# Kernel tuning notes

Measured on AMD Instinct MI355X. Metric: run time of the kernel, lower is better.

## Reference

```python
import jax, jax.numpy as jnp
import numpy as np

H, D = 16, 64  # heads, dim_head


def _rope(x):
    # x: (b, h, n, d). rotary-embedding-torch style: interleaved pairs, theta=10000.
    n, d = x.shape[-2], x.shape[-1]
    inv_freq = 1.0 / (10000.0 ** (jnp.arange(0, d, 2, dtype=jnp.float32) / d))  # (d/2,)
    ang = jnp.arange(n, dtype=jnp.float32)[:, None] * inv_freq[None, :]  # (n, d/2)
    cos = jnp.repeat(jnp.cos(ang), 2, axis=-1).astype(x.dtype)  # (n, d) interleaved
    sin = jnp.repeat(jnp.sin(ang), 2, axis=-1).astype(x.dtype)
    xp = x.reshape(*x.shape[:-1], d // 2, 2)
    rot = jnp.stack((-xp[..., 1], xp[..., 0]), axis=-1).reshape(x.shape)
    return x * cos + rot * sin


def setup_inputs() -> dict:
    key = jax.random.key(0)
    k1, k2, k3 = jax.random.split(key, 3)
    b, n, dim = 2, 2048, 1024
    inner = H * D
    x = jax.random.normal(k1, (b, n, dim), jnp.float32)
    w_qkv = jax.random.normal(k2, (dim, 3 * inner), jnp.float32) / np.sqrt(dim).astype(np.float32)
    w_out = jax.random.normal(k3, (inner, dim), jnp.float32) / np.sqrt(inner).astype(np.float32)
    b_out = jnp.zeros((dim,), jnp.float32)
    return {"x": x, "w_qkv": w_qkv, "w_out": w_out, "b_out": b_out}


def reference(x, w_qkv, w_out, b_out):
    b, n, _ = x.shape
    qkv = x @ w_qkv  # (b, n, 3*H*D)
    q, k, v = jnp.split(qkv, 3, axis=-1)

    def split_heads(t):
        return t.reshape(b, n, H, D).transpose(0, 2, 1, 3)  # (b, h, n, d)

    q, k, v = split_heads(q), split_heads(k), split_heads(v)
    q = _rope(q)
    k = _rope(k)
    scale = 1.0 / jnp.sqrt(jnp.asarray(D, dtype=x.dtype))
    scores = jnp.einsum('bhqd,bhkd->bhqk', q, k) * scale
    attn = jax.nn.softmax(scores, axis=-1)
    o = jnp.einsum('bhqk,bhkd->bhqd', attn, v)
    o = o.transpose(0, 2, 1, 3).reshape(b, n, H * D)
    return o @ w_out + b_out
```

## Files before the change

kernel.cpp:

```cpp
#include <hip/hip_runtime.h>
#include <math.h>

#define B_    2
#define N_    2048
#define DIM_  1024
#define H_    16
#define D_    64
#define INNER_ 1024
#define QKVC_ 3072

typedef __attribute__((ext_vector_type(8))) short short8;
typedef __attribute__((ext_vector_type(4))) short short4v;
typedef __attribute__((ext_vector_type(4))) float f32x4;
typedef __attribute__((ext_vector_type(4))) float float4v;
typedef _Float16 half8 __attribute__((ext_vector_type(8)));
typedef __fp16 fp16v2 __attribute__((ext_vector_type(2)));

union h8u { short8 s; half8 h; fp16v2 h2[4]; };
static __device__ __forceinline__ half8 s2h(short8 s) { h8u u; u.s = s; return u.h; }

static __device__ __forceinline__ unsigned short f2h(float f) {
    _Float16 h = (_Float16)f;
    unsigned short u;
    __builtin_memcpy(&u, &h, 2);
    return u;
}

static __device__ __forceinline__ void gload16(const void* g, void* l) {
    __builtin_amdgcn_global_load_lds((__attribute__((address_space(1))) void*)(g),
                                     (__attribute__((address_space(3))) void*)(l),
                                     16, 0, 0);
}

__global__ __launch_bounds__(256) void convert_all(const float* __restrict__ X,
                                                   const float* __restrict__ Wq,
                                                   const float* __restrict__ Wo,
                                                   unsigned short* __restrict__ Xh,
                                                   unsigned short* __restrict__ WqT,
                                                   unsigned short* __restrict__ WoT) {
    __shared__ unsigned short Sh[64][65];
    const int blk = blockIdx.x;
    const int tid = threadIdx.x;
    if (blk < 2048) {
        int t = blk * 256 + tid;
        size_t off = (size_t)t * 8;
        float4v a = *(const float4v*)(X + off);
        float4v b = *(const float4v*)(X + off + 4);
        short8 o;
#pragma unroll
        for (int j = 0; j < 4; ++j) {
            o[j]     = (short)f2h(a[j]);
            o[4 + j] = (short)f2h(b[j]);
        }
        *(short8*)(Xh + off) = o;
        return;
    }
    const float* W;
    unsigned short* T;
    int n0, k0, Nw;
    if (blk < 2816) {
        int g = blk - 2048;
        W = Wq; T = WqT; Nw = QKVC_;
        n0 = (g % 48) * 64; k0 = (g / 48) * 64;
    } else {
        int g = blk - 2816;
        W = Wo; T = WoT; Nw = DIM_;
        n0 = (g % 16) * 64; k0 = (g / 16) * 64;
    }
#pragma unroll
    for (int l = 0; l < 16; ++l) {
        int idx = tid + l * 256;
        int r = idx >> 6, c = idx & 63;
        Sh[c][r] = f2h(W[(size_t)(k0 + r) * Nw + n0 + c]);
    }
    __syncthreads();
#pragma unroll
    for (int l = 0; l < 16; ++l) {
        int idx = tid + l * 256;
        int r = idx >> 6, c = idx & 63;
        T[(size_t)(n0 + r) * 1024 + k0 + c] = Sh[r][c];
    }
}

#define GEMM_STAGE64(gA, gB)                                                       \
    {                                                                              \
        int srow = lane >> 3;                                                      \
        int gsw  = ((lane & 7) ^ srow) * 8;                                        \
        _Pragma("unroll") for (int i_ = 0; i_ < 4; ++i_) {                         \
            gload16(gA + (size_t)(m0 + w * 32 + 8 * i_ + srow) * 1024 + k0 + gsw,  \
                    sA + (w * 32 + 8 * i_) * 64);                                  \
            gload16(gB + (size_t)(n0 + w * 32 + 8 * i_ + srow) * 1024 + k0 + gsw,  \
                    sB + (w * 32 + 8 * i_) * 64);                                  \
        }                                                                          \
    }

#define GEMM_BODY64()                                                              \
    half8 af[4][2], bf[4][2];                                                      \
    _Pragma("unroll") for (int f = 0; f < 4; ++f) {                                \
        int arow = (wr + f * 16 + (lane & 15)) * 64;                               \
        int brow = (wc + f * 16 + (lane & 15)) * 64;                               \
        _Pragma("unroll") for (int h = 0; h < 2; ++h) {                            \
            int g = (((lane >> 4) + 4 * h) ^ (lane & 7)) * 8;                      \
            af[f][h] = s2h(*(const short8*)&sA[arow + g]);                         \
            bf[f][h] = s2h(*(const short8*)&sB[brow + g]);                         \
        }                                                                          \
    }                                                                              \
    _Pragma("unroll") for (int i = 0; i < 4; ++i)                                  \
        _Pragma("unroll") for (int j = 0; j < 4; ++j) {                            \
            acc[i][j] = __builtin_amdgcn_mfma_f32_16x16x32_f16(af[i][0], bf[j][0], acc[i][j], 0, 0, 0); \
            acc[i][j] = __builtin_amdgcn_mfma_f32_16x16x32_f16(af[i][1], bf[j][1], acc[i][j], 0, 0, 0); \
        }

#define XCD_REMAP()                                                                \
    const int fblk = blockIdx.y * gridDim.x + blockIdx.x;                          \
    const int per_ = (gridDim.x * gridDim.y) >> 3;                                 \
    const int rf = (fblk & 7) * per_ + (fblk >> 3);                                \
    const int m0 = (rf / gridDim.x) * 128, n0 = (rf % gridDim.x) * 128;

#define QSCALE 0.180336879963f
__global__ __launch_bounds__(256) void qkv_gemm_mfma(const unsigned short* __restrict__ Ah,
                                                     const unsigned short* __restrict__ Bh,
                                                     unsigned short* __restrict__ Qh,
                                                     unsigned short* __restrict__ Kh,
                                                     unsigned short* __restrict__ Vh) {
    __shared__ __align__(16) unsigned short sA[8192], sB[8192];
    const int tid = threadIdx.x;
    const int lane = tid & 63, w = tid >> 6;
    const int wr = (w >> 1) * 64, wc = (w & 1) * 64;
    XCD_REMAP();
    f32x4 acc[4][4] = {};

    for (int k0 = 0; k0 < 1024; k0 += 64) {
        GEMM_STAGE64(Ah, Bh);
        __syncthreads();
        GEMM_BODY64();
        __syncthreads();
    }

    const int seg = n0 >> 10;
    const int parity = lane & 1;

#pragma unroll
    for (int i = 0; i < 4; ++i) {
        int mbase = m0 + wr + i * 16 + (lane >> 4) * 4;
#pragma unroll
        for (int j = 0; j < 4; ++j) {
            int col = n0 + wc + j * 16 + (lane & 15);
            int wcol = col & 1023;
            int h = wcol >> 6, dd = wcol & 63;
            unsigned short* dst = (seg == 0) ? Qh : (seg == 1 ? Kh : Vh);
            if (seg == 2) {
#pragma unroll
                for (int r = 0; r < 4; ++r) {
                    int row = mbase + r;
                    int b = row >> 11, n = row & (N_ - 1);
                    dst[((size_t)(b * H_ + h) * N_ + n) * D_ + dd] = f2h(acc[i][j][r]);
                }
            } else {
                float freq = __builtin_amdgcn_exp2f((float)(dd >> 1) * -0.4152410118f);
#pragma unroll
                for (int r = 0; r < 4; ++r) {
                    int row = mbase + r;
                    int b = row >> 11, n = row & (N_ - 1);
                    float ang = (float)n * freq;
                    float s = __sinf(ang);
                    float c = __cosf(ang);
                    float val = acc[i][j][r];
                    float partner = __shfl_xor(val, 1);
                    float rot = parity ? (val * c + partner * s)
                                       : (val * c - partner * s);
                    if (seg == 0) rot *= QSCALE;
                    dst[((size_t)(b * H_ + h) * N_ + n) * D_ + dd] = f2h(rot);
                }
            }
        }
    }
}

__global__ __launch_bounds__(256) void out_gemm_mfma(const unsigned short* __restrict__ Ah,
                                                     const unsigned short* __restrict__ Bh,
                                                     const float* __restrict__ bias,
                                                     float* __restrict__ C) {
    __shared__ __align__(16) unsigned short sA[8192], sB[4096];
    const int tid = threadIdx.x;
    const int lane = tid & 63, w = tid >> 6;
    const int wr = w * 32;
    const int fblk = blockIdx.y * gridDim.x + blockIdx.x;
    const int per_ = (gridDim.x * gridDim.y) >> 3;
    const int rf = (fblk & 7) * per_ + (fblk >> 3);
    const int m0 = (rf / gridDim.x) * 128, n0 = (rf % gridDim.x) * 64;
    f32x4 acc[2][4] = {};

    for (int k0 = 0; k0 < 1024; k0 += 64) {
        {
            int srow = lane >> 3;
            int gsw  = ((lane & 7) ^ srow) * 8;
#pragma unroll
            for (int i_ = 0; i_ < 4; ++i_)
                gload16(Ah + (size_t)(m0 + w * 32 + 8 * i_ + srow) * 1024 + k0 + gsw,
                        sA + (w * 32 + 8 * i_) * 64);
            gload16(Bh + (size_t)(n0 + w * 8 + srow) * 1024 + k0 + gsw,
                    sB + (w * 8) * 64);
            gload16(Bh + (size_t)(n0 + 32 + w * 8 + srow) * 1024 + k0 + gsw,
                    sB + (32 + w * 8) * 64);
        }
        __syncthreads();
        {
            half8 af[2][2], bf[4][2];
#pragma unroll
            for (int f = 0; f < 2; ++f) {
                int arow = (wr + f * 16 + (lane & 15)) * 64;
#pragma unroll
                for (int h = 0; h < 2; ++h) {
                    int g = (((lane >> 4) + 4 * h) ^ (lane & 7)) * 8;
                    af[f][h] = s2h(*(const short8*)&sA[arow + g]);
                }
            }
#pragma unroll
            for (int j = 0; j < 4; ++j) {
                int brow = (j * 16 + (lane & 15)) * 64;
#pragma unroll
                for (int h = 0; h < 2; ++h) {
                    int g = (((lane >> 4) + 4 * h) ^ (lane & 7)) * 8;
                    bf[j][h] = s2h(*(const short8*)&sB[brow + g]);
                }
            }
#pragma unroll
            for (int i = 0; i < 2; ++i)
#pragma unroll
                for (int j = 0; j < 4; ++j) {
                    acc[i][j] = __builtin_amdgcn_mfma_f32_16x16x32_f16(af[i][0], bf[j][0], acc[i][j], 0, 0, 0);
                    acc[i][j] = __builtin_amdgcn_mfma_f32_16x16x32_f16(af[i][1], bf[j][1], acc[i][j], 0, 0, 0);
                }
        }
        __syncthreads();
    }

#pragma unroll
    for (int i = 0; i < 2; ++i) {
        int mbase = m0 + wr + i * 16 + (lane >> 4) * 4;
#pragma unroll
        for (int j = 0; j < 4; ++j) {
            int col = n0 + j * 16 + (lane & 15);
            float bv = bias[col];
#pragma unroll
            for (int r = 0; r < 4; ++r)
                C[(size_t)(mbase + r) * DIM_ + col] = acc[i][j][r] + bv;
        }
    }
}

#define PADV 72
#define NT   (N_ / 64)
__global__ __launch_bounds__(1024, 2) void attn_mfma(const unsigned short* __restrict__ Qh,
                                                     const unsigned short* __restrict__ Kh,
                                                     const unsigned short* __restrict__ Vh,
                                                     unsigned short* __restrict__ Oh) {
    __shared__ __align__(16) unsigned short Ks[2 * 64 * 64];
    __shared__ __align__(16) unsigned short Vt[3][64][PADV];
    const int tid = threadIdx.x;
    const int w = tid >> 6;
    const int l = tid & 63;
    const int lr = l & 15, lg = l >> 4;
    const bool stager = (tid < 512);

    const int f = blockIdx.y * gridDim.x + blockIdx.x;
    const int x = f & 7, g = f >> 3;
    const int bh = x * 4 + (g >> 3);
    const int q0 = (g & 7) * 256;
    const size_t base = (size_t)bh * N_ * D_;

    const int srow = tid >> 3;
    const int scg  = tid & 7;
    const int gcg  = scg ^ (srow & 7);
    const unsigned short* ksrc = Kh + base + (size_t)srow * D_ + gcg * 8;
    unsigned short* kdst = Ks + w * 512;

    const int kb0 = lr * 64 + (lg ^ (lr & 7)) * 8;
    const int kb1 = lr * 64 + ((lg + 4) ^ (lr & 7)) * 8;

    const int sd0 = (tid & 15) * 4;
    const int skv = ((tid >> 4) & 31) * 2;
    const int vpos = ((skv >> 5) * 32) + (((skv >> 2) & 3) * 8) +
                     (((skv >> 4) & 1) * 4) + (skv & 3);

    const unsigned short* qrow = Qh + base + (size_t)(q0 + w * 16 + lr) * D_ + lg * 8;
    const half8 qf0 = s2h(*(const short8*)qrow);
    const half8 qf1 = s2h(*(const short8*)(qrow + 32));

    f32x4 oacc[4] = {};
    float lsum = 0.f;
    h8u pa_prev[2];
    pa_prev[0].s = short8{0,0,0,0,0,0,0,0};
    pa_prev[1].s = short8{0,0,0,0,0,0,0,0};

    if (stager) {
        gload16(ksrc, kdst);
        short4v r0 = *(const short4v*)(Vh + base + (size_t)(skv + 0) * D_ + sd0);
        short4v r1 = *(const short4v*)(Vh + base + (size_t)(skv + 1) * D_ + sd0);
#pragma unroll
        for (int j = 0; j < 4; ++j) {
            unsigned int pk = (unsigned int)(unsigned short)r0[j] |
                              ((unsigned int)(unsigned short)r1[j] << 16);
            *(unsigned int*)&Vt[0][sd0 + j][vpos] = pk;
        }
    }

    int rd = 2, cu = 0, wr_ = 1;

    for (int ti = 0; ti < NT; ++ti) {
        const int kcur = ti & 1, knxt = kcur ^ 1;
        __syncthreads();

        short4v n0v = {}, n1v = {};
        if (stager && ti + 1 < NT) {
            gload16(ksrc + (size_t)(ti + 1) * 64 * D_, kdst + knxt * 4096);
            const unsigned short* nsrc = Vh + base + (size_t)((ti + 1) * 64 + skv) * D_ + sd0;
            n0v = *(const short4v*)nsrc;
            n1v = *(const short4v*)(nsrc + D_);
        }

        f32x4 sacc[4] = {};
        const unsigned short* kbuf = Ks + kcur * 4096;
        __builtin_amdgcn_s_setprio(1);
#pragma unroll
        for (int t = 0; t < 4; ++t) {
            half8 kf0 = s2h(*(const short8*)(kbuf + t * 1024 + kb0));
            half8 kf1 = s2h(*(const short8*)(kbuf + t * 1024 + kb1));
            sacc[t] = __builtin_amdgcn_mfma_f32_16x16x32_f16(kf0, qf0, sacc[t], 0, 0, 0);
            sacc[t] = __builtin_amdgcn_mfma_f32_16x16x32_f16(kf1, qf1, sacc[t], 0, 0, 0);
        }
        if (ti > 0) {
#pragma unroll
            for (int m2 = 0; m2 < 2; ++m2)
#pragma unroll
                for (int dt = 0; dt < 4; ++dt) {
                    half8 vf = s2h(*(const short8*)&Vt[rd][dt * 16 + lr][m2 * 32 + lg * 8]);
                    oacc[dt] = __builtin_amdgcn_mfma_f32_16x16x32_f16(pa_prev[m2].h, vf, oacc[dt], 0, 0, 0);
                }
        }
        __builtin_amdgcn_s_setprio(0);

#pragma unroll
        for (int t = 0; t < 4; ++t) {
            float e0 = __builtin_amdgcn_exp2f(sacc[t][0]);
            float e1 = __builtin_amdgcn_exp2f(sacc[t][1]);
            float e2 = __builtin_amdgcn_exp2f(sacc[t][2]);
            float e3 = __builtin_amdgcn_exp2f(sacc[t][3]);
            lsum += (e0 + e1) + (e2 + e3);
            pa_prev[t >> 1].h2[(t & 1) * 2]     = __builtin_amdgcn_cvt_pkrtz(e0, e1);
            pa_prev[t >> 1].h2[(t & 1) * 2 + 1] = __builtin_amdgcn_cvt_pkrtz(e2, e3);
        }

        if (stager && ti + 1 < NT) {
#pragma unroll
            for (int j = 0; j < 4; ++j) {
                unsigned int pk = (unsigned int)(unsigned short)n0v[j] |
                                  ((unsigned int)(unsigned short)n1v[j] << 16);
                *(unsigned int*)&Vt[wr_][sd0 + j][vpos] = pk;
            }
        }
        int t_ = rd; rd = cu; cu = wr_; wr_ = t_;
    }

#pragma unroll
    for (int m2 = 0; m2 < 2; ++m2)
#pragma unroll
        for (int dt = 0; dt < 4; ++dt) {
            half8 vf = s2h(*(const short8*)&Vt[rd][dt * 16 + lr][m2 * 32 + lg * 8]);
            oacc[dt] = __builtin_amdgcn_mfma_f32_16x16x32_f16(pa_prev[m2].h, vf, oacc[dt], 0, 0, 0);
        }

    lsum += __shfl_xor(lsum, 16);
    lsum += __shfl_xor(lsum, 32);
    int b = bh >> 4, h = bh & 15;
#pragma unroll
    for (int r = 0; r < 4; ++r) {
        float ls = __shfl(lsum, lg * 4 + r);
        float inv = 1.0f / ls;
        size_t orow = ((size_t)b * N_ + q0 + w * 16 + lg * 4 + r) * INNER_ + h * 64 + lr;
#pragma unroll
        for (int dt = 0; dt < 4; ++dt)
            Oh[orow + 16 * dt] = f2h(oacc[dt][r] * inv);
    }
}

extern "C" void kernel_launch(void* const* d_in, const int* in_sizes, int n_in,
                              void* d_out, int out_size, void* d_ws, size_t ws_size,
                              hipStream_t stream) {
    const float* x     = (const float*)d_in[0];
    const float* w_qkv = (const float*)d_in[1];
    const float* w_out = (const float*)d_in[2];
    const float* b_out = (const float*)d_in[3];
    float* out = (float*)d_out;

    unsigned short* Xh  = (unsigned short*)d_ws;
    unsigned short* WqT = Xh + 4194304;
    unsigned short* WoT = WqT + 3145728;
    unsigned short* Qh  = WoT + 1048576;
    unsigned short* Kh  = Qh + 4194304;
    unsigned short* Vh  = Kh + 4194304;

    convert_all<<<dim3(3072), 256, 0, stream>>>(x, w_qkv, w_out, Xh, WqT, WoT);
    qkv_gemm_mfma<<<dim3(QKVC_ / 128, 32), 256, 0, stream>>>(Xh, WqT, Qh, Kh, Vh);
    attn_mfma<<<dim3(8, 32), 1024, 0, stream>>>(Qh, Kh, Vh, Xh);
    out_gemm_mfma<<<dim3(DIM_ / 64, 32), 256, 0, stream>>>(Xh, WoT, b_out, out);
}
```

Measured before the change: 112.6 us.

## Split attention over two KV halves and add a combine kernel

```diff
diff --git a/kernel.cpp b/kernel.cpp
--- a/kernel.cpp
+++ b/kernel.cpp
@@ -24,6 +24,11 @@
     unsigned short u;
     __builtin_memcpy(&u, &h, 2);
     return u;
+}
+static __device__ __forceinline__ float h2f(unsigned short u) {
+    _Float16 h;
+    __builtin_memcpy(&h, &u, 2);
+    return (float)h;
 }
 
 static __device__ __forceinline__ void gload16(const void* g, void* l) {
@@ -252,10 +257,14 @@
 
 #define PADV 72
 #define NT   (N_ / 64)
+#define NTH  (NT / 2)
 __global__ __launch_bounds__(1024, 2) void attn_mfma(const unsigned short* __restrict__ Qh,
                                                      const unsigned short* __restrict__ Kh,
                                                      const unsigned short* __restrict__ Vh,
-                                                     unsigned short* __restrict__ Oh) {
+                                                     unsigned short* __restrict__ O0h,
+                                                     unsigned short* __restrict__ O1h,
+                                                     float* __restrict__ L0,
+                                                     float* __restrict__ L1) {
     __shared__ __align__(16) unsigned short Ks[2 * 64 * 64];
     __shared__ __align__(16) unsigned short Vt[3][64][PADV];
     const int tid = threadIdx.x;
@@ -266,9 +275,14 @@
 
     const int f = blockIdx.y * gridDim.x + blockIdx.x;
     const int x = f & 7, g = f >> 3;
-    const int bh = x * 4 + (g >> 3);
-    const int q0 = (g & 7) * 256;
+    const int bh = x * 4 + (g >> 4);
+    const int rem = g & 15;
+    const int q0 = (rem >> 1) * 256;
+    const int half = rem & 1;
+    const int t0 = half * NTH;
     const size_t base = (size_t)bh * N_ * D_;
+    unsigned short* Ohalf = half ? O1h : O0h;
+    float* Lh = half ? L1 : L0;
 
     const int srow = tid >> 3;
     const int scg  = tid & 7;
@@ -295,9 +309,9 @@
     pa_prev[1].s = short8{0,0,0,0,0,0,0,0};
 
     if (stager) {
-        gload16(ksrc, kdst);
-        short4v r0 = *(const short4v*)(Vh + base + (size_t)(skv + 0) * D_ + sd0);
-        short4v r1 = *(const short4v*)(Vh + base + (size_t)(skv + 1) * D_ + sd0);
+        gload16(ksrc + (size_t)t0 * 64 * D_, kdst);
+        short4v r0 = *(const short4v*)(Vh + base + (size_t)(t0 * 64 + skv + 0) * D_ + sd0);
+        short4v r1 = *(const short4v*)(Vh + base + (size_t)(t0 * 64 + skv + 1) * D_ + sd0);
 #pragma unroll
         for (int j = 0; j < 4; ++j) {
             unsigned int pk = (unsigned int)(unsigned short)r0[j] |
@@ -308,12 +322,13 @@
 
     int rd = 2, cu = 0, wr_ = 1;
 
-    for (int ti = 0; ti < NT; ++ti) {
-        const int kcur = ti & 1, knxt = kcur ^ 1;
+    for (int it = 0; it < NTH; ++it) {
+        const int ti = t0 + it;
+        const int kcur = it & 1, knxt = kcur ^ 1;
         __syncthreads();
 
         short4v n0v = {}, n1v = {};
-        if (stager && ti + 1 < NT) {
+        if (stager && it + 1 < NTH) {
             gload16(ksrc + (size_t)(ti + 1) * 64 * D_, kdst + knxt * 4096);
             const unsigned short* nsrc = Vh + base + (size_t)((ti + 1) * 64 + skv) * D_ + sd0;
             n0v = *(const short4v*)nsrc;
@@ -330,7 +345,7 @@
             sacc[t] = __builtin_amdgcn_mfma_f32_16x16x32_f16(kf0, qf0, sacc[t], 0, 0, 0);
             sacc[t] = __builtin_amdgcn_mfma_f32_16x16x32_f16(kf1, qf1, sacc[t], 0, 0, 0);
         }
-        if (ti > 0) {
+        if (it > 0) {
 #pragma unroll
             for (int m2 = 0; m2 < 2; ++m2)
 #pragma unroll
@@ -352,7 +367,7 @@
             pa_prev[t >> 1].h2[(t & 1) * 2 + 1] = __builtin_amdgcn_cvt_pkrtz(e2, e3);
         }
 
-        if (stager && ti + 1 < NT) {
+        if (stager && it + 1 < NTH) {
 #pragma unroll
             for (int j = 0; j < 4; ++j) {
                 unsigned int pk = (unsigned int)(unsigned short)n0v[j] |
@@ -373,16 +388,39 @@
 
     lsum += __shfl_xor(lsum, 16);
     lsum += __shfl_xor(lsum, 32);
+    if (lg == 0)
+        Lh[(size_t)bh * N_ + q0 + w * 16 + lr] = lsum;
+
     int b = bh >> 4, h = bh & 15;
 #pragma unroll
     for (int r = 0; r < 4; ++r) {
-        float ls = __shfl(lsum, lg * 4 + r);
-        float inv = 1.0f / ls;
         size_t orow = ((size_t)b * N_ + q0 + w * 16 + lg * 4 + r) * INNER_ + h * 64 + lr;
 #pragma unroll
         for (int dt = 0; dt < 4; ++dt)
-            Oh[orow + 16 * dt] = f2h(oacc[dt][r] * inv);
-    }
+            Ohalf[orow + 16 * dt] = f2h(oacc[dt][r]);
+    }
+}
+
+__global__ __launch_bounds__(256) void attn_combine(const unsigned short* __restrict__ O0h,
+                                                    const unsigned short* __restrict__ O1h,
+                                                    const float* __restrict__ L0,
+                                                    const float* __restrict__ L1,
+                                                    unsigned short* __restrict__ Oh) {
+    int t = blockIdx.x * blockDim.x + threadIdx.x;
+    size_t e = (size_t)t * 8;
+    int row = (int)(e >> 10);
+    int col = (int)(e & 1023);
+    int h = col >> 6;
+    int b = row >> 11, n = row & (N_ - 1);
+    size_t lidx = (size_t)(b * H_ + h) * N_ + n;
+    float inv = 1.0f / (L0[lidx] + L1[lidx]);
+    short8 a = *(const short8*)(O0h + e);
+    short8 c = *(const short8*)(O1h + e);
+    short8 o;
+#pragma unroll
+    for (int j = 0; j < 8; ++j)
+        o[j] = (short)f2h((h2f((unsigned short)a[j]) + h2f((unsigned short)c[j])) * inv);
+    *(short8*)(Oh + e) = o;
 }
 
 extern "C" void kernel_launch(void* const* d_in, const int* in_sizes, int n_in,
@@ -400,9 +438,14 @@
     unsigned short* Qh  = WoT + 1048576;
     unsigned short* Kh  = Qh + 4194304;
     unsigned short* Vh  = Kh + 4194304;
+    unsigned short* O0h = Vh + 4194304;
+    unsigned short* O1h = O0h + 4194304;
+    float* L0 = (float*)(O1h + 4194304);
+    float* L1 = L0 + 65536;
 
     convert_all<<<dim3(3072), 256, 0, stream>>>(x, w_qkv, w_out, Xh, WqT, WoT);
     qkv_gemm_mfma<<<dim3(QKVC_ / 128, 32), 256, 0, stream>>>(Xh, WqT, Qh, Kh, Vh);
-    attn_mfma<<<dim3(8, 32), 1024, 0, stream>>>(Qh, Kh, Vh, Xh);
+    attn_mfma<<<dim3(16, 32), 1024, 0, stream>>>(Qh, Kh, Vh, O0h, O1h, L0, L1);
+    attn_combine<<<dim3(2048), 256, 0, stream>>>(O0h, O1h, L0, L1, Xh);
     out_gemm_mfma<<<dim3(DIM_ / 64, 32), 256, 0, stream>>>(Xh, WoT, b_out, out);
 }
```

Measured after the change: 232.2 us. 2.06x slower.
